# Performance work log

Hardware: AMD Instinct MI355X
Metric: run time of the kernel (lower is better)

Reference implementation:

```python
import jax, jax.numpy as jnp
import numpy as np

N = 10000        # nodes
E = 160000       # edges (avg degree 16)
MUL = 128        # channel multiplicity
A = 10           # node-attr (species one-hot) dim
RAD = 8          # radial bessel features
INV_SQRT3 = 0.5773502691896258  # CG coefficient for 1o x 1o -> 0e


def _mlp(x, Ws):
    # RadialMLP: linear layers with SiLU between, no activation on last
    for W in Ws[:-1]:
        x = jax.nn.silu(x @ W)
    return x @ Ws[-1]


def setup_inputs() -> dict:
    key = jax.random.key(0)
    ks = jax.random.split(key, 25)

    def g(k, shape):
        return jax.random.normal(k, shape, jnp.float32) / np.float32(np.sqrt(shape[0]))

    return {
        "node_attrs": jax.random.uniform(ks[0], (N, A), jnp.float32),
        "node_feats": jax.random.normal(ks[1], (N, 4 * MUL), jnp.float32),
        "edge_attrs": jax.random.normal(ks[2], (E, 4), jnp.float32),
        "edge_feats": jax.random.uniform(ks[3], (E, RAD), jnp.float32),
        "W_src": g(ks[5], (A, MUL)),
        "W_tgt": g(ks[6], (A, MUL)),
        "W_up0": g(ks[7], (MUL, MUL)),
        "W_up1": g(ks[8], (MUL, MUL)),
        "W_skip0": g(ks[9], (MUL, MUL)),
        "W_skip1": g(ks[10], (MUL, MUL)),
        "W_res0": g(ks[11], (MUL, 2 * MUL)),
        "W_res1": g(ks[12], (MUL, MUL)),
        "W_lin1_0": g(ks[13], (2 * MUL, 2 * MUL)),
        "W_lin1_1": g(ks[14], (2 * MUL, MUL)),
        "W_lin2_0": g(ks[15], (MUL, MUL)),
        "W_lin2_1": g(ks[16], (MUL, MUL)),
        "W_rad1": g(ks[17], (RAD + 2 * MUL, 64)),
        "W_rad2": g(ks[18], (64, 64)),
        "W_rad3": g(ks[19], (64, 64)),
        "W_rad4": g(ks[20], (64, 4 * MUL)),
        "W_den1": g(ks[21], (RAD + 2 * MUL, 64)),
        "W_den2": g(ks[22], (64, 1)),
        "alpha": jnp.ones((), jnp.float32),   # scaled by 20 inside (alpha = param * 20)
        "beta": jnp.zeros((), jnp.float32),
        "edge_index": jax.random.randint(ks[4], (E, 2), 0, N),
    }


def _forward(node_attrs, node_feats, edge_attrs, edge_feats,
             W_src, W_tgt, W_up0, W_up1, W_skip0, W_skip1, W_res0, W_res1,
             W_lin1_0, W_lin1_1, W_lin2_0, W_lin2_1,
             W_rad1, W_rad2, W_rad3, W_rad4, W_den1, W_den2,
             alpha, beta, edge_index):
    n = node_feats.shape[0]
    # split node feats into 128x0e scalars and 128x1o vectors (mul_ir layout)
    s = node_feats[:, :MUL]                           # [N, 128]
    v = node_feats[:, MUL:].reshape(n, MUL, 3)        # [N, 128, 3]

    # skip connection: Linear(node_feats_irreps -> hidden_irreps)
    sc_s = s @ W_skip0
    sc_v = jnp.einsum("nui,uv->nvi", v, W_skip1)
    sc = jnp.concatenate([sc_s, sc_v.reshape(n, -1)], axis=-1)  # [N, 512]

    # linear_up (node_feats -> edge_irreps) and linear_res (-> irreps_nonlin)
    up_s = s @ W_up0
    up_v = jnp.einsum("nui,uv->nvi", v, W_up1)
    res_s = s @ W_res0                                # [N, 256] (scalars + gates)
    res_v = jnp.einsum("nui,uv->nvi", v, W_res1)      # [N, 128, 3]

    # per-species scalar embeddings, gathered per edge
    src_emb = node_attrs @ W_src                      # [N, 128]
    tgt_emb = node_attrs @ W_tgt
    snd = edge_index[:, 0]
    rcv = edge_index[:, 1]
    aug = jnp.concatenate([edge_feats, src_emb[snd], tgt_emb[rcv]], axis=-1)  # [E, 264]

    # radial MLP -> per-edge tensor-product weights; density MLP
    tpw = _mlp(aug, [W_rad1, W_rad2, W_rad3, W_rad4])  # [E, 512]
    edge_density = jnp.tanh(_mlp(aug, [W_den1, W_den2]) ** 2)  # [E, 1]
    density = jax.ops.segment_sum(edge_density, rcv, num_segments=n)  # [N, 1]

    # equivariant tensor product (uvu, per-edge weights), lmax=1 CG paths
    xs = up_s[snd]                                    # [E, 128]
    xv = up_v[snd]                                    # [E, 128, 3]
    y0 = edge_attrs[:, :1]                            # [E, 1]
    y1 = edge_attrs[:, 1:4]                           # [E, 3]
    wA, wB, wC, wD = jnp.split(tpw, 4, axis=-1)
    mA = wA * xs * y0                                               # 0e x 0e -> 0e
    mD = wD * jnp.einsum("eui,ei->eu", xv, y1) * INV_SQRT3          # 1o x 1o -> 0e
    mB = (wB * xs)[:, :, None] * y1[:, None, :]                     # 0e x 1o -> 1o
    mC = wC[:, :, None] * xv * y0[:, :, None]                       # 1o x 0e -> 1o
    m_s = jnp.concatenate([mA, mD], axis=-1)          # [E, 256]
    m_v = jnp.concatenate([mB, mC], axis=1)           # [E, 256, 3]

    # scatter-add messages to receiver nodes
    msg_s = jax.ops.segment_sum(m_s, rcv, num_segments=n)  # [N, 256]
    msg_v = jax.ops.segment_sum(m_v, rcv, num_segments=n)  # [N, 256, 3]

    # linear_1 (irreps_mid -> irreps_nonlin), density normalization, residual
    msg_s = msg_s @ W_lin1_0                          # [N, 256]
    msg_v = jnp.einsum("nui,uv->nvi", msg_v, W_lin1_1)  # [N, 128, 3]
    denom = density * beta + alpha * 20.0             # [N, 1]
    msg_s = msg_s / denom + res_s
    msg_v = msg_v / denom[..., None] + res_v

    # equivariant gate nonlinearity: silu on scalars, sigmoid gates on vectors
    scal = jax.nn.silu(msg_s[:, :MUL])
    gate = jax.nn.sigmoid(msg_s[:, MUL:])
    vec = msg_v * gate[:, :, None]

    # linear_2 and reshape to [N, channels, (lmax+1)^2]
    out_s = scal @ W_lin2_0                           # [N, 128]
    out_v = jnp.einsum("nui,uv->nvi", vec, W_lin2_1)  # [N, 128, 3]
    message = jnp.concatenate([out_s[:, :, None], out_v], axis=-1)  # [N, 128, 4]
    return message, sc


def reference(node_attrs, node_feats, edge_attrs, edge_feats,
              W_src, W_tgt, W_up0, W_up1, W_skip0, W_skip1, W_res0, W_res1,
              W_lin1_0, W_lin1_1, W_lin2_0, W_lin2_1,
              W_rad1, W_rad2, W_rad3, W_rad4, W_den1, W_den2,
              alpha, beta, edge_index):
    return _forward(node_attrs, node_feats, edge_attrs, edge_feats,
                    W_src, W_tgt, W_up0, W_up1, W_skip0, W_skip1, W_res0, W_res1,
                    W_lin1_0, W_lin1_1, W_lin2_0, W_lin2_1,
                    W_rad1, W_rad2, W_rad3, W_rad4, W_den1, W_den2,
                    alpha, beta, edge_index)
```

## Files before the change

### kernel.cpp

```cpp
#include <hip/hip_runtime.h>
#include <math.h>

#define NN 10000
#define NE 160000
#define MUL 128
#define ADIM 10
#define RADF 8
#define HID 64
#define INV_SQRT3 0.57735026918962576f
#define NB64 157

typedef __attribute__((ext_vector_type(8))) short bf16x8;
typedef __attribute__((ext_vector_type(4))) float f32x4;

__device__ __forceinline__ float silu_f(float x){ return x / (1.0f + __expf(-x)); }
__device__ __forceinline__ float sigmoid_f(float x){ return 1.0f / (1.0f + __expf(-x)); }
__device__ __forceinline__ unsigned short f2b(float f){
  union{float f; unsigned u;} v; v.f=f;
  unsigned r = (v.u + 0x7fffu + ((v.u>>16)&1u))>>16;
  return (unsigned short)r;
}
__device__ __forceinline__ float b2f(unsigned short h){
  union{unsigned u; float f;} v; v.u = ((unsigned)h)<<16; return v.f;
}
__device__ __forceinline__ float b2f_lo(unsigned u){
  union{unsigned u; float f;} v; v.u = u<<16; return v.f;
}
__device__ __forceinline__ float b2f_hi(unsigned u){
  union{unsigned u; float f;} v; v.u = u & 0xffff0000u; return v.f;
}

__global__ __launch_bounds__(256) void k_wcomb(
    const float* __restrict__ Wsrc, const float* __restrict__ Wtgt,
    const float* __restrict__ Wr1, const float* __restrict__ Wd1,
    float* __restrict__ Wc){
  int tid = threadIdx.x;
  int m = tid>>6, c = tid&63;
  const float* WA = (m&1)? Wtgt : Wsrc;
  const float* WB = (m<2)? Wr1 : Wd1;
  int koff = (m&1)? 136 : 8;
  for (int a=0;a<ADIM;a++){
    float s=0.f;
    for (int k=0;k<128;k++) s += WA[a*128+k]*WB[(koff+k)*64+c];
    Wc[(m*ADIM+a)*64+c] = s;
  }
}

__global__ __launch_bounds__(256) void k_nodeemb(
    const float* __restrict__ attrs, const float* __restrict__ Wc,
    float* __restrict__ srP, float* __restrict__ trP,
    float* __restrict__ sdP, float* __restrict__ tdP){
  int idx = blockIdx.x*256 + threadIdx.x;
  if (idx >= NN*64) return;
  int n = idx>>6, c = idx&63;
  float s0=0,s1=0,s2=0,s3=0;
  #pragma unroll
  for (int a=0;a<ADIM;a++){
    float x = attrs[n*ADIM+a];
    s0 += x*Wc[(0*ADIM+a)*64+c];
    s1 += x*Wc[(1*ADIM+a)*64+c];
    s2 += x*Wc[(2*ADIM+a)*64+c];
    s3 += x*Wc[(3*ADIM+a)*64+c];
  }
  srP[idx]=s0; trP[idx]=s1; sdP[idx]=s2; tdP[idx]=s3;
}

__global__ __launch_bounds__(256) void k_feat_prep(
    const float* __restrict__ feats, unsigned short* __restrict__ fs16,
    unsigned short* __restrict__ fv16){
  int idx = blockIdx.x*256 + threadIdx.x;
  int n = idx >> 9, c = idx & 511;
  float v = feats[idx];
  if (c < 128) fs16[n*128 + c] = f2b(v);
  else {
    int q = c - 128; int u = q/3; int i = q - 3*u;
    fv16[((size_t)n*3 + i)*128 + u] = f2b(v);
  }
}

__global__ __launch_bounds__(256) void k_prep(
    const float* __restrict__ Wr2, const float* __restrict__ Wr3,
    const float* __restrict__ Wr4,
    const float* __restrict__ Wl10, const float* __restrict__ Wl11,
    const float* __restrict__ Wl20, const float* __restrict__ Wl21,
    const float* __restrict__ Wsk0, const float* __restrict__ Wup0, const float* __restrict__ Wres0,
    const float* __restrict__ Wsk1, const float* __restrict__ Wup1, const float* __restrict__ Wres1,
    unsigned short* __restrict__ WTr2, unsigned short* __restrict__ WTr3,
    unsigned short* __restrict__ WTr4,
    unsigned short* __restrict__ Wl10T, unsigned short* __restrict__ Wl11T,
    unsigned short* __restrict__ Wl20T, unsigned short* __restrict__ Wl21T,
    unsigned short* __restrict__ WnsT, unsigned short* __restrict__ WnvT){
  int idx = blockIdx.x*256 + threadIdx.x;
  if (idx < 4096){
    int j = idx; int n=j>>6, k=j&63;
    WTr2[j] = f2b(Wr2[k*64+n]);
  } else if (idx < 8192){
    int j = idx-4096; int n=j>>6, k=j&63;
    WTr3[j] = f2b(Wr3[k*64+n]);
  } else if (idx < 40960){
    int j = idx-8192; int n=j>>6, k=j&63;
    WTr4[j] = f2b(Wr4[k*512+n]);
  } else if (idx < 106496){
    int j = idx-40960; int n=j>>8, k=j&255;
    Wl10T[j] = f2b(Wl10[k*256+n]);
  } else if (idx < 139264){
    int j = idx-106496; int n=j>>8, k=j&255;
    Wl11T[j] = f2b(Wl11[k*128+n]);
  } else if (idx < 155648){
    int j = idx-139264; int n=j>>7, k=j&127;
    Wl20T[j] = f2b(Wl20[k*128+n]);
  } else if (idx < 172032){
    int j = idx-155648; int n=j>>7, k=j&127;
    Wl21T[j] = f2b(Wl21[k*128+n]);
  } else if (idx < 237568){
    int j = idx-172032; int n=j>>7, k=j&127;
    float v;
    if (n < 128)      v = Wsk0[k*128+n];
    else if (n < 256) v = Wup0[k*128+(n-128)];
    else              v = Wres0[k*256+(n-256)];
    WnsT[j] = f2b(v);
  } else if (idx < 286720){
    int j = idx-237568; int n=j>>7, k=j&127;
    float v;
    if (n < 128)      v = Wsk1[k*128+n];
    else if (n < 256) v = Wup1[k*128+(n-128)];
    else              v = Wres1[k*128+(n-256)];
    WnvT[j] = f2b(v);
  }
}

__global__ __launch_bounds__(256) void k_node_pre2(
    const unsigned short* __restrict__ fs16, const unsigned short* __restrict__ fv16,
    const unsigned short* __restrict__ WnsT, const unsigned short* __restrict__ WnvT,
    float* __restrict__ out_sc,
    unsigned* __restrict__ up_sp, unsigned* __restrict__ up_vp,
    float* __restrict__ res_s, float* __restrict__ res_v){
  __shared__ unsigned short fA[64][136];
  int nb = blockIdx.x*64;
  int c = blockIdx.y;
  int g, ntc;
  if (c < 4){ g=0; ntc=c; } else { g = 1 + (c-4)/3; ntc = (c-4)%3; }
  int tid = threadIdx.x;
  int w = tid>>6, l = tid&63, m0 = w*16, lr = l&15, lg = l>>4;
  for (int idx=tid; idx<64*16; idx+=256){
    int row = idx>>4, s8 = idx&15;
    int n = min(nb+row, NN-1);
    const unsigned short* src = (g==0) ? &fs16[(size_t)n*128 + s8*8]
                                       : &fv16[((size_t)n*3 + (g-1))*128 + s8*8];
    *(uint4*)&fA[row][s8*8] = *(const uint4*)src;
  }
  __syncthreads();
  const unsigned short* WT = ((g==0)? WnsT : WnvT) + (size_t)ntc*128*128;
  f32x4 acc[8];
  #pragma unroll
  for (int t=0;t<8;t++) acc[t]=(f32x4)(0.f);
  #pragma unroll
  for (int kb=0;kb<4;kb++){
    bf16x8 a = *(const bf16x8*)&fA[m0+lr][kb*32 + lg*8];
    #pragma unroll
    for (int t=0;t<8;t++){
      bf16x8 b = *(const bf16x8*)&WT[(size_t)(t*16+lr)*128 + kb*32 + lg*8];
      acc[t] = __builtin_amdgcn_mfma_f32_16x16x32_bf16(a, b, acc[t], 0,0,0);
    }
  }
  #pragma unroll
  for (int t=0;t<8;t++){
    #pragma unroll
    for (int r=0;r<4;r++){
      int col = (ntc*8+t)*16 + lr;
      int row = m0 + lg*4 + r;
      int n = nb + row;
      if (n < NN){
        float v = acc[t][r];
        if (g==0){
          if (col < 128)      out_sc[(size_t)n*512 + col] = v;
          else if (col < 256){
            int cc = col-128;
            ((unsigned short*)up_sp)[((size_t)n*64 + (cc&63))*2 + (cc>>6)] = f2b(v);
          } else              res_s[(size_t)n*256 + col-256] = v;
        } else {
          int i = g-1;
          if (col < 128)      out_sc[(size_t)n*512 + 128 + col*3 + i] = v;
          else if (col < 256){
            int cc = col-128;
            ((unsigned short*)up_vp)[(((size_t)n*3+i)*64 + (cc&63))*2 + (cc>>6)] = f2b(v);
          } else              res_v[((size_t)n*3+i)*128 + col-256] = v;
        }
      }
    }
  }
}

__global__ __launch_bounds__(256) void k_deg(const int* __restrict__ eidx, int* __restrict__ deg){
  int i = blockIdx.x*256+threadIdx.x;
  if (i<NE) atomicAdd(&deg[eidx[2*i+1]],1);
}
__global__ __launch_bounds__(256) void k_scan(const int* __restrict__ deg, int* __restrict__ offsets){
  __shared__ int part[256];
  int t = threadIdx.x; int base = t*40;
  int s=0;
  for (int k=0;k<40;k++){ int idx=base+k; if (idx<NN) s+=deg[idx]; }
  part[t]=s; __syncthreads();
  if (t==0){ int run=0; for (int i=0;i<256;i++){ int v=part[i]; part[i]=run; run+=v; } }
  __syncthreads();
  int run = part[t];
  for (int k=0;k<40;k++){
    int idx=base+k;
    if (idx<=NN) offsets[idx]=run;
    if (idx<NN) run+=deg[idx];
  }
}
__global__ __launch_bounds__(256) void k_fill(const int* __restrict__ eidx, const int* __restrict__ offsets,
                                              int* __restrict__ cursor, int* __restrict__ elist){
  int i = blockIdx.x*256+threadIdx.x;
  if (i<NE){ int r = eidx[2*i+1]; int p = atomicAdd(&cursor[r],1); elist[offsets[r]+p]=i; }
}

__global__ __launch_bounds__(256) void k_tpw(
    const int* __restrict__ elist, const int* __restrict__ eidx,
    const float* __restrict__ ef, const float* __restrict__ ea,
    const float* __restrict__ srP, const float* __restrict__ trP,
    const float* __restrict__ sdP, const float* __restrict__ tdP,
    const float* __restrict__ Wr1, const float* __restrict__ Wd1, const float* __restrict__ Wd2,
    const unsigned short* __restrict__ WTr2, const unsigned short* __restrict__ WTr3,
    const unsigned short* __restrict__ WTr4,
    const int* __restrict__ offsets, int nstart, int nend, int cap,
    unsigned* __restrict__ tpwp, float4* __restrict__ ybuf,
    int* __restrict__ sndbuf, float* __restrict__ densbuf){
  __shared__ unsigned short hA[64][72];
  __shared__ unsigned short hB[64][72];
  __shared__ unsigned short hC[64][72];
  __shared__ float efs[64][8];
  __shared__ int s_snd[64], s_rcv[64];
  int ebase = offsets[nstart];
  int eend  = min(offsets[nend], ebase + cap);
  int i0 = ebase + blockIdx.x*64;
  if (i0 >= eend) return;
  int nrows = min(64, eend - i0);
  int tid = threadIdx.x;
  int w = tid>>6, l = tid&63, m0 = w*16, lr = l&15, lg = l>>4;
  if (tid < 64){
    int ii = min(i0 + tid, eend-1);
    int e = elist[ii];
    int sn = eidx[2*e], rc = eidx[2*e+1];
    s_snd[tid]=sn; s_rcv[tid]=rc;
    if (tid < nrows){
      int li = i0 - ebase + tid;
      sndbuf[li] = sn;
      ybuf[li] = ((const float4*)ea)[e];
    }
  }
  if (tid < 128){
    int r = tid>>1, hf = tid&1;
    int e = elist[min(i0+r, eend-1)];
    *(float4*)&efs[r][hf*4] = *(const float4*)&ef[(size_t)e*8 + hf*4];
  }
  __syncthreads();
  {
    float wr[8], wd[8];
    #pragma unroll
    for (int k=0;k<8;k++){ wr[k]=Wr1[k*64+l]; wd[k]=Wd1[k*64+l]; }
    float wd2c = Wd2[l];
    #pragma unroll
    for (int j=0;j<16;j++){
      int r = m0+j;
      int sn = s_snd[r], rc = s_rcv[r];
      float h  = srP[sn*64+l] + trP[rc*64+l];
      float hd = sdP[sn*64+l] + tdP[rc*64+l];
      #pragma unroll
      for (int k=0;k<8;k++){ float ek=efs[r][k]; h += ek*wr[k]; hd += ek*wd[k]; }
      hA[r][l] = f2b(silu_f(h));
      float sv = silu_f(hd)*wd2c;
      #pragma unroll
      for (int m=32;m;m>>=1) sv += __shfl_xor(sv, m);
      if (l==0 && j+m0 < nrows) densbuf[i0 - ebase + r] = tanhf(sv*sv);
    }
  }
  f32x4 acc[4];
  #pragma unroll
  for (int nt=0;nt<4;nt++) acc[nt]=(f32x4)(0.f);
  for (int kb=0;kb<2;kb++){
    bf16x8 a = *(const bf16x8*)&hA[m0+lr][kb*32 + lg*8];
    #pragma unroll
    for (int nt=0;nt<4;nt++){
      bf16x8 b = *(const bf16x8*)&WTr2[(nt*16+lr)*64 + kb*32 + lg*8];
      acc[nt] = __builtin_amdgcn_mfma_f32_16x16x32_bf16(a, b, acc[nt], 0,0,0);
    }
  }
  #pragma unroll
  for (int nt=0;nt<4;nt++)
    #pragma unroll
    for (int r=0;r<4;r++)
      hB[m0+lg*4+r][nt*16+lr] = f2b(silu_f(acc[nt][r]));
  #pragma unroll
  for (int nt=0;nt<4;nt++) acc[nt]=(f32x4)(0.f);
  for (int kb=0;kb<2;kb++){
    bf16x8 a = *(const bf16x8*)&hB[m0+lr][kb*32 + lg*8];
    #pragma unroll
    for (int nt=0;nt<4;nt++){
      bf16x8 b = *(const bf16x8*)&WTr3[(nt*16+lr)*64 + kb*32 + lg*8];
      acc[nt] = __builtin_amdgcn_mfma_f32_16x16x32_bf16(a, b, acc[nt], 0,0,0);
    }
  }
  #pragma unroll
  for (int nt=0;nt<4;nt++)
    #pragma unroll
    for (int r=0;r<4;r++)
      hA[m0+lg*4+r][nt*16+lr] = f2b(silu_f(acc[nt][r]));
  int li0 = i0 - ebase + m0;
  (void)li0;
  for (int G=0; G<4; G++){
    f32x4 aE[4], aO[4];
    #pragma unroll
    for (int nt=0;nt<4;nt++){ aE[nt]=(f32x4)(0.f); aO[nt]=(f32x4)(0.f); }
    for (int kb=0;kb<2;kb++){
      bf16x8 a = *(const bf16x8*)&hA[m0+lr][kb*32 + lg*8];
      #pragma unroll
      for (int nt=0;nt<4;nt++){
        bf16x8 bE = *(const bf16x8*)&WTr4[((2*G)*64+nt*16+lr)*64 + kb*32 + lg*8];
        bf16x8 bO = *(const bf16x8*)&WTr4[((2*G+1)*64+nt*16+lr)*64 + kb*32 + lg*8];
        aE[nt] = __builtin_amdgcn_mfma_f32_16x16x32_bf16(a, bE, aE[nt], 0,0,0);
        aO[nt] = __builtin_amdgcn_mfma_f32_16x16x32_bf16(a, bO, aO[nt], 0,0,0);
      }
    }
    #pragma unroll
    for (int nt=0;nt<4;nt++)
      #pragma unroll
      for (int r=0;r<4;r++){
        hB[m0+lg*4+r][nt*16+lr] = f2b(aE[nt][r]);
        hC[m0+lg*4+r][nt*16+lr] = f2b(aO[nt][r]);
      }
    {
      int row = m0 + (l>>2), seg = l&3;
      if (row < nrows){
        const unsigned short* pb = &hB[row][seg*16];
        const unsigned short* pc = &hC[row][seg*16];
        unsigned o[16];
        #pragma unroll
        for (int t=0;t<16;t++) o[t] = (unsigned)pb[t] | ((unsigned)pc[t]<<16);
        size_t base = (size_t)(i0 - ebase + row)*256 + G*64 + seg*16;
        *(uint4*)&tpwp[base+0]  = *(uint4*)&o[0];
        *(uint4*)&tpwp[base+4]  = *(uint4*)&o[4];
        *(uint4*)&tpwp[base+8]  = *(uint4*)&o[8];
        *(uint4*)&tpwp[base+12] = *(uint4*)&o[12];
      }
    }
  }
}

__global__ __launch_bounds__(256) void k_gather(
    const unsigned* __restrict__ tpwp, const float4* __restrict__ ybuf,
    const int* __restrict__ sndbuf, const float* __restrict__ densbuf,
    const unsigned* __restrict__ up_sp, const unsigned* __restrict__ up_vp,
    const int* __restrict__ offsets, int nstart,
    unsigned short* __restrict__ msg_s16, unsigned short* __restrict__ msg_v16,
    float* __restrict__ density){
  int w = threadIdx.x>>6, l = threadIdx.x&63;
  int n = nstart + blockIdx.x*4 + w;
  if (n >= NN) return;
  int ebase = offsets[nstart];
  int s0 = offsets[n], s1 = offsets[n+1];
  float mA0=0,mA1=0,mD0=0,mD1=0;
  float mB00=0,mB01=0,mB10=0,mB11=0,mB20=0,mB21=0;
  float mC00=0,mC01=0,mC10=0,mC11=0,mC20=0,mC21=0;
  float dsum=0;
  #pragma unroll 2
  for (int i=s0;i<s1;++i){
    int li = i - ebase;
    int sn = sndbuf[li];
    float4 y = ybuf[li];
    dsum += densbuf[li];
    const unsigned* tp = tpwp + (size_t)li*256;
    unsigned uA = tp[l], uB = tp[64+l], uC = tp[128+l], uD = tp[192+l];
    float wA0=b2f_lo(uA), wA1=b2f_hi(uA);
    float wB0=b2f_lo(uB), wB1=b2f_hi(uB);
    float wC0=b2f_lo(uC), wC1=b2f_hi(uC);
    float wD0=b2f_lo(uD), wD1=b2f_hi(uD);
    unsigned us = up_sp[(size_t)sn*64 + l];
    float xs0=b2f_lo(us), xs1=b2f_hi(us);
    unsigned uv0 = up_vp[((size_t)sn*3+0)*64 + l];
    unsigned uv1 = up_vp[((size_t)sn*3+1)*64 + l];
    unsigned uv2 = up_vp[((size_t)sn*3+2)*64 + l];
    float xv00=b2f_lo(uv0), xv01=b2f_hi(uv0);
    float xv10=b2f_lo(uv1), xv11=b2f_hi(uv1);
    float xv20=b2f_lo(uv2), xv21=b2f_hi(uv2);
    mA0 += wA0*xs0*y.x; mA1 += wA1*xs1*y.x;
    float dot0 = xv00*y.y + xv10*y.z + xv20*y.w;
    float dot1 = xv01*y.y + xv11*y.z + xv21*y.w;
    mD0 += wD0*dot0; mD1 += wD1*dot1;
    float b0 = wB0*xs0, b1 = wB1*xs1;
    mB00 += b0*y.y; mB01 += b1*y.y;
    mB10 += b0*y.z; mB11 += b1*y.z;
    mB20 += b0*y.w; mB21 += b1*y.w;
    float c0 = wC0*y.x, c1 = wC1*y.x;
    mC00 += c0*xv00; mC01 += c1*xv01;
    mC10 += c0*xv10; mC11 += c1*xv11;
    mC20 += c0*xv20; mC21 += c1*xv21;
  }
  unsigned short* ms = msg_s16 + (size_t)n*256;
  ms[l]=f2b(mA0); ms[64+l]=f2b(mA1);
  ms[128+l]=f2b(mD0*INV_SQRT3); ms[192+l]=f2b(mD1*INV_SQRT3);
  unsigned short* mv = msg_v16 + (size_t)n*768;
  mv[l]=f2b(mB00);     mv[64+l]=f2b(mB01);  mv[128+l]=f2b(mC00); mv[192+l]=f2b(mC01);
  mv[256+l]=f2b(mB10); mv[320+l]=f2b(mB11); mv[384+l]=f2b(mC10); mv[448+l]=f2b(mC11);
  mv[512+l]=f2b(mB20); mv[576+l]=f2b(mB21); mv[640+l]=f2b(mC20); mv[704+l]=f2b(mC21);
  if (l==0) density[n]=dsum;
}

__global__ __launch_bounds__(256) void k_post1(
    const unsigned short* __restrict__ msg_s16, const unsigned short* __restrict__ msg_v16,
    const float* __restrict__ density,
    const float* __restrict__ res_s, const float* __restrict__ res_v,
    const unsigned short* __restrict__ Wl10T, const unsigned short* __restrict__ Wl11T,
    const float* __restrict__ alphap, const float* __restrict__ betap,
    unsigned short* __restrict__ scal16, unsigned short* __restrict__ gate16,
    unsigned short* __restrict__ vtmp16){
  __shared__ unsigned short sm[64][264];
  __shared__ float sden[64];
  int nb = blockIdx.x*64, y = blockIdx.y;
  int tid = threadIdx.x;
  int w = tid>>6, l = tid&63, m0 = w*16, lr = l&15, lg = l>>4;
  for (int idx=tid; idx<64*32; idx+=256){
    int row = idx>>5, s8 = idx&31;
    int n = min(nb+row, NN-1);
    const unsigned short* src = (y<2)? &msg_s16[(size_t)n*256 + s8*8]
                                     : &msg_v16[(size_t)n*768 + (y-2)*256 + s8*8];
    *(uint4*)&sm[row][s8*8] = *(const uint4*)src;
  }
  if (tid < 64){
    int n = min(nb+tid, NN-1);
    sden[tid] = density[n]*betap[0] + alphap[0]*20.0f;
  }
  __syncthreads();
  const unsigned short* BT = (y<2)? (Wl10T + (size_t)y*128*256) : Wl11T;
  f32x4 acc[8];
  #pragma unroll
  for (int t=0;t<8;t++) acc[t]=(f32x4)(0.f);
  for (int kb=0;kb<8;kb++){
    bf16x8 a = *(const bf16x8*)&sm[m0+lr][kb*32 + lg*8];
    #pragma unroll
    for (int t=0;t<8;t++){
      bf16x8 b = *(const bf16x8*)&BT[(size_t)(t*16+lr)*256 + kb*32 + lg*8];
      acc[t] = __builtin_amdgcn_mfma_f32_16x16x32_bf16(a, b, acc[t], 0,0,0);
    }
  }
  #pragma unroll
  for (int t=0;t<8;t++){
    #pragma unroll
    for (int r=0;r<4;r++){
      int col = t*16+lr;
      int row = m0 + lg*4 + r;
      int n = nb + row;
      if (n < NN){
        float v = acc[t][r]/sden[row];
        if (y==0){
          v += res_s[(size_t)n*256 + col];
          scal16[(size_t)n*128 + col] = f2b(silu_f(v));
        } else if (y==1){
          v += res_s[(size_t)n*256 + 128 + col];
          gate16[(size_t)n*128 + col] = f2b(sigmoid_f(v));
        } else {
          int i = y-2;
          v += res_v[((size_t)n*3+i)*128 + col];
          vtmp16[((size_t)i*NN + n)*128 + col] = f2b(v);
        }
      }
    }
  }
}

__global__ __launch_bounds__(256) void k_post2(
    const unsigned short* __restrict__ scal16, const unsigned short* __restrict__ gate16,
    const unsigned short* __restrict__ vtmp16,
    const unsigned short* __restrict__ Wl20T, const unsigned short* __restrict__ Wl21T,
    float* __restrict__ out_msg){
  __shared__ unsigned short sA[64][136];
  int nb = blockIdx.x*64, y = blockIdx.y;
  int tid = threadIdx.x;
  int w = tid>>6, l = tid&63, m0 = w*16, lr = l&15, lg = l>>4;
  for (int idx=tid; idx<64*16; idx+=256){
    int row = idx>>4, s8 = idx&15;
    int n = min(nb+row, NN-1);
    if (y==0){
      *(uint4*)&sA[row][s8*8] = *(const uint4*)&scal16[(size_t)n*128 + s8*8];
    } else {
      int i = y-1;
      uint4 va = *(const uint4*)&vtmp16[((size_t)i*NN + n)*128 + s8*8];
      uint4 vg = *(const uint4*)&gate16[(size_t)n*128 + s8*8];
      const unsigned short* pa = (const unsigned short*)&va;
      const unsigned short* pg = (const unsigned short*)&vg;
      unsigned short o[8];
      #pragma unroll
      for (int j=0;j<8;j++) o[j] = f2b(b2f(pa[j])*b2f(pg[j]));
      *(uint4*)&sA[row][s8*8] = *(const uint4*)o;
    }
  }
  __syncthreads();
  const unsigned short* BT = (y==0)? Wl20T : Wl21T;
  f32x4 acc[8];
  #pragma unroll
  for (int t=0;t<8;t++) acc[t]=(f32x4)(0.f);
  #pragma unroll
  for (int kb=0;kb<4;kb++){
    bf16x8 a = *(const bf16x8*)&sA[m0+lr][kb*32 + lg*8];
    #pragma unroll
    for (int t=0;t<8;t++){
      bf16x8 b = *(const bf16x8*)&BT[(size_t)(t*16+lr)*128 + kb*32 + lg*8];
      acc[t] = __builtin_amdgcn_mfma_f32_16x16x32_bf16(a, b, acc[t], 0,0,0);
    }
  }
  #pragma unroll
  for (int t=0;t<8;t++){
    #pragma unroll
    for (int r=0;r<4;r++){
      int col = t*16+lr;
      int n = nb + m0 + lg*4 + r;
      if (n < NN) out_msg[(size_t)n*512 + col*4 + y] = acc[t][r];
    }
  }
}

extern "C" void kernel_launch(void* const* d_in, const int* in_sizes, int n_in,
                              void* d_out, int out_size, void* d_ws, size_t ws_size,
                              hipStream_t stream){
  (void)in_sizes; (void)n_in; (void)out_size;
  const float* attrs = (const float*)d_in[0];
  const float* feats = (const float*)d_in[1];
  const float* ea    = (const float*)d_in[2];
  const float* ef    = (const float*)d_in[3];
  const float* Wsrc  = (const float*)d_in[4];
  const float* Wtgt  = (const float*)d_in[5];
  const float* Wup0  = (const float*)d_in[6];
  const float* Wup1  = (const float*)d_in[7];
  const float* Wsk0  = (const float*)d_in[8];
  const float* Wsk1  = (const float*)d_in[9];
  const float* Wres0 = (const float*)d_in[10];
  const float* Wres1 = (const float*)d_in[11];
  const float* Wl10  = (const float*)d_in[12];
  const float* Wl11  = (const float*)d_in[13];
  const float* Wl20  = (const float*)d_in[14];
  const float* Wl21  = (const float*)d_in[15];
  const float* Wr1   = (const float*)d_in[16];
  const float* Wr2   = (const float*)d_in[17];
  const float* Wr3   = (const float*)d_in[18];
  const float* Wr4   = (const float*)d_in[19];
  const float* Wd1   = (const float*)d_in[20];
  const float* Wd2   = (const float*)d_in[21];
  const float* alphap= (const float*)d_in[22];
  const float* betap = (const float*)d_in[23];
  const int*   eidx  = (const int*)d_in[24];

  const size_t fixed_bytes =
      (size_t)NN*256*2 + (size_t)NN*768*2 + (size_t)NN*256*4 + (size_t)NN*384*4 +
      (size_t)NN*4 + (size_t)NN*64*4 + (size_t)NN*192*4 +
      (size_t)NN*128*2 + (size_t)NN*384*2 +
      4*(size_t)NN*64*4 + 4*ADIM*64*4 + (size_t)NN*128*2 +
      (4096+4096+32768+65536+32768+16384+16384+65536+49152)*2 +
      (10240+10240+10256)*4 + (size_t)NE*4 + 64*256;
  int nchunk, npc, cap;
  if (fixed_bytes + (size_t)NE*1048 + 65536 <= ws_size){ nchunk=1; npc=NN;   cap=NE;    }
  else if (fixed_bytes + 81920ULL*1048 + 65536 <= ws_size){ nchunk=2; npc=5000; cap=81920; }
  else { nchunk=4; npc=2500; cap=44032; }

  char* p = (char*)d_ws;
  auto alloc = [&](size_t bytes)->char*{ char* r=p; p += (bytes+255)&~(size_t)255; return r; };
  unsigned* tpwp  = (unsigned*)alloc((size_t)cap*256*4);
  unsigned short* msg_s16 = (unsigned short*)alloc((size_t)NN*256*2);
  unsigned short* msg_v16 = (unsigned short*)alloc((size_t)NN*768*2);
  float*  res_s   = (float*)alloc((size_t)NN*256*4);
  float*  res_v   = (float*)alloc((size_t)NN*384*4);
  float*  density = (float*)alloc((size_t)NN*4);
  float4* ybuf    = (float4*)alloc((size_t)cap*16);
  float*  densbuf = (float*)alloc((size_t)cap*4);
  int*    sndbuf  = (int*)alloc((size_t)cap*4);
  unsigned* up_sp = (unsigned*)alloc((size_t)NN*64*4);
  unsigned* up_vp = (unsigned*)alloc((size_t)NN*192*4);
  unsigned short* fs16 = (unsigned short*)alloc((size_t)NN*128*2);
  unsigned short* fv16 = (unsigned short*)alloc((size_t)NN*384*2);
  float* srP = (float*)alloc((size_t)NN*64*4);
  float* trP = (float*)alloc((size_t)NN*64*4);
  float* sdP = (float*)alloc((size_t)NN*64*4);
  float* tdP = (float*)alloc((size_t)NN*64*4);
  float* Wc  = (float*)alloc(4*ADIM*64*4);
  unsigned short* gate16 = (unsigned short*)alloc((size_t)NN*128*2);
  unsigned short* WTr2 = (unsigned short*)alloc(4096*2);
  unsigned short* WTr3 = (unsigned short*)alloc(4096*2);
  unsigned short* WTr4 = (unsigned short*)alloc(32768*2);
  unsigned short* Wl10T = (unsigned short*)alloc(65536*2);
  unsigned short* Wl11T = (unsigned short*)alloc(32768*2);
  unsigned short* Wl20T = (unsigned short*)alloc(16384*2);
  unsigned short* Wl21T = (unsigned short*)alloc(16384*2);
  unsigned short* WnsT  = (unsigned short*)alloc(65536*2);
  unsigned short* WnvT  = (unsigned short*)alloc(49152*2);
  int* deg     = (int*)alloc(10240*4);
  int* cursor  = (int*)alloc(10240*4);
  int* offsets = (int*)alloc(10256*4);
  int* elist   = (int*)alloc((size_t)NE*4);

  unsigned short* scal16 = fs16;
  unsigned short* vtmp16 = fv16;

  float* out_msg = (float*)d_out;
  float* out_sc  = out_msg + (size_t)NN*512;

  hipMemsetAsync(deg, 0, 2*10240*sizeof(int), stream);

  k_wcomb<<<1, 256, 0, stream>>>(Wsrc, Wtgt, Wr1, Wd1, Wc);
  k_prep<<<1120, 256, 0, stream>>>(Wr2, Wr3, Wr4, Wl10, Wl11, Wl20, Wl21,
                                   Wsk0, Wup0, Wres0, Wsk1, Wup1, Wres1,
                                   WTr2, WTr3, WTr4,
                                   Wl10T, Wl11T, Wl20T, Wl21T, WnsT, WnvT);
  k_nodeemb<<<(NN*64+255)/256, 256, 0, stream>>>(attrs, Wc, srP, trP, sdP, tdP);
  k_feat_prep<<<NN*512/256, 256, 0, stream>>>(feats, fs16, fv16);
  k_node_pre2<<<dim3(NB64,13), 256, 0, stream>>>(fs16, fv16, WnsT, WnvT,
                                                 out_sc, up_sp, up_vp, res_s, res_v);
  k_deg<<<(NE+255)/256, 256, 0, stream>>>(eidx, deg);
  k_scan<<<1, 256, 0, stream>>>(deg, offsets);
  k_fill<<<(NE+255)/256, 256, 0, stream>>>(eidx, offsets, cursor, elist);

  int tpw_blocks = (cap+63)/64;
  for (int c=0; c<nchunk; ++c){
    k_tpw<<<tpw_blocks, 256, 0, stream>>>(elist, eidx, ef, ea,
                                          srP, trP, sdP, tdP,
                                          Wr1, Wd1, Wd2, WTr2, WTr3, WTr4,
                                          offsets, c*npc, (c+1)*npc, cap,
                                          tpwp, ybuf, sndbuf, densbuf);
    k_gather<<<npc/4, 256, 0, stream>>>(tpwp, ybuf, sndbuf, densbuf, up_sp, up_vp,
                                        offsets, c*npc, msg_s16, msg_v16, density);
  }

  k_post1<<<dim3(NB64,5), 256, 0, stream>>>(msg_s16, msg_v16, density, res_s, res_v,
                                            Wl10T, Wl11T, alphap, betap,
                                            scal16, gate16, vtmp16);
  k_post2<<<dim3(NB64,4), 256, 0, stream>>>(scal16, gate16, vtmp16,
                                            Wl20T, Wl21T, out_msg);
}
```

Baseline: 464.1 us.

## Interleave per-node and per-edge buffers for vector loads in edge kernels

Node embedding projections are interleaved into two float2-packed arrays, one for sender terms and one for receiver terms. The up-projected node features are packed into one 16-byte record per node and channel pair, and the per-edge tensor-product weights are written in a channel-interleaved layout. Together these let the gather kernel fetch each edge's weights and sender features with one uint4 load apiece instead of eight scattered 32-bit loads, and the radial MLP kernel now writes its output straight from registers without a shared-memory staging buffer. The weight-combine kernel is folded into the prep kernel, which removes one launch but runs its serial 128-term loop inside a single extra block.

```diff
diff --git a/kernel.cpp b/kernel.cpp
--- a/kernel.cpp
+++ b/kernel.cpp
@@ -30,26 +30,9 @@
   union{unsigned u; float f;} v; v.u = u & 0xffff0000u; return v.f;
 }
 
-__global__ __launch_bounds__(256) void k_wcomb(
-    const float* __restrict__ Wsrc, const float* __restrict__ Wtgt,
-    const float* __restrict__ Wr1, const float* __restrict__ Wd1,
-    float* __restrict__ Wc){
-  int tid = threadIdx.x;
-  int m = tid>>6, c = tid&63;
-  const float* WA = (m&1)? Wtgt : Wsrc;
-  const float* WB = (m<2)? Wr1 : Wd1;
-  int koff = (m&1)? 136 : 8;
-  for (int a=0;a<ADIM;a++){
-    float s=0.f;
-    for (int k=0;k<128;k++) s += WA[a*128+k]*WB[(koff+k)*64+c];
-    Wc[(m*ADIM+a)*64+c] = s;
-  }
-}
-
 __global__ __launch_bounds__(256) void k_nodeemb(
     const float* __restrict__ attrs, const float* __restrict__ Wc,
-    float* __restrict__ srP, float* __restrict__ trP,
-    float* __restrict__ sdP, float* __restrict__ tdP){
+    float* __restrict__ pA, float* __restrict__ pB){
   int idx = blockIdx.x*256 + threadIdx.x;
   if (idx >= NN*64) return;
   int n = idx>>6, c = idx&63;
@@ -62,7 +45,10 @@
     s2 += x*Wc[(2*ADIM+a)*64+c];
     s3 += x*Wc[(3*ADIM+a)*64+c];
   }
-  srP[idx]=s0; trP[idx]=s1; sdP[idx]=s2; tdP[idx]=s3;
+  pA[(size_t)n*128 + c*2 + 0] = s0;
+  pA[(size_t)n*128 + c*2 + 1] = s2;
+  pB[(size_t)n*128 + c*2 + 0] = s1;
+  pB[(size_t)n*128 + c*2 + 1] = s3;
 }
 
 __global__ __launch_bounds__(256) void k_feat_prep(
@@ -85,11 +71,14 @@
     const float* __restrict__ Wl20, const float* __restrict__ Wl21,
     const float* __restrict__ Wsk0, const float* __restrict__ Wup0, const float* __restrict__ Wres0,
     const float* __restrict__ Wsk1, const float* __restrict__ Wup1, const float* __restrict__ Wres1,
+    const float* __restrict__ Wsrc, const float* __restrict__ Wtgt,
+    const float* __restrict__ Wr1, const float* __restrict__ Wd1,
     unsigned short* __restrict__ WTr2, unsigned short* __restrict__ WTr3,
     unsigned short* __restrict__ WTr4,
     unsigned short* __restrict__ Wl10T, unsigned short* __restrict__ Wl11T,
     unsigned short* __restrict__ Wl20T, unsigned short* __restrict__ Wl21T,
-    unsigned short* __restrict__ WnsT, unsigned short* __restrict__ WnvT){
+    unsigned short* __restrict__ WnsT, unsigned short* __restrict__ WnvT,
+    float* __restrict__ Wc){
   int idx = blockIdx.x*256 + threadIdx.x;
   if (idx < 4096){
     int j = idx; int n=j>>6, k=j&63;
@@ -126,6 +115,17 @@
     else if (n < 256) v = Wup1[k*128+(n-128)];
     else              v = Wres1[k*128+(n-256)];
     WnvT[j] = f2b(v);
+  } else if (idx < 286976){
+    int j = idx - 286720;
+    int m = j>>6, c = j&63;
+    const float* WA = (m&1)? Wtgt : Wsrc;
+    const float* WB = (m<2)? Wr1 : Wd1;
+    int koff = (m&1)? 136 : 8;
+    for (int a=0;a<ADIM;a++){
+      float s=0.f;
+      for (int k=0;k<128;k++) s += WA[a*128+k]*WB[(koff+k)*64+c];
+      Wc[(m*ADIM+a)*64+c] = s;
+    }
   }
 }
 
@@ -133,7 +133,7 @@
     const unsigned short* __restrict__ fs16, const unsigned short* __restrict__ fv16,
     const unsigned short* __restrict__ WnsT, const unsigned short* __restrict__ WnvT,
     float* __restrict__ out_sc,
-    unsigned* __restrict__ up_sp, unsigned* __restrict__ up_vp,
+    unsigned short* __restrict__ upk16,
     float* __restrict__ res_s, float* __restrict__ res_v){
   __shared__ unsigned short fA[64][136];
   int nb = blockIdx.x*64;
@@ -176,14 +176,14 @@
           if (col < 128)      out_sc[(size_t)n*512 + col] = v;
           else if (col < 256){
             int cc = col-128;
-            ((unsigned short*)up_sp)[((size_t)n*64 + (cc&63))*2 + (cc>>6)] = f2b(v);
+            upk16[(size_t)n*512 + (cc&63)*8 + (cc>>6)] = f2b(v);
           } else              res_s[(size_t)n*256 + col-256] = v;
         } else {
           int i = g-1;
           if (col < 128)      out_sc[(size_t)n*512 + 128 + col*3 + i] = v;
           else if (col < 256){
             int cc = col-128;
-            ((unsigned short*)up_vp)[(((size_t)n*3+i)*64 + (cc&63))*2 + (cc>>6)] = f2b(v);
+            upk16[(size_t)n*512 + (cc&63)*8 + (1+i)*2 + (cc>>6)] = f2b(v);
           } else              res_v[((size_t)n*3+i)*128 + col-256] = v;
         }
       }
@@ -219,8 +219,7 @@
 __global__ __launch_bounds__(256) void k_tpw(
     const int* __restrict__ elist, const int* __restrict__ eidx,
     const float* __restrict__ ef, const float* __restrict__ ea,
-    const float* __restrict__ srP, const float* __restrict__ trP,
-    const float* __restrict__ sdP, const float* __restrict__ tdP,
+    const float* __restrict__ pA, const float* __restrict__ pB,
     const float* __restrict__ Wr1, const float* __restrict__ Wd1, const float* __restrict__ Wd2,
     const unsigned short* __restrict__ WTr2, const unsigned short* __restrict__ WTr3,
     const unsigned short* __restrict__ WTr4,
@@ -229,7 +228,6 @@
     int* __restrict__ sndbuf, float* __restrict__ densbuf){
   __shared__ unsigned short hA[64][72];
   __shared__ unsigned short hB[64][72];
-  __shared__ unsigned short hC[64][72];
   __shared__ float efs[64][8];
   __shared__ int s_snd[64], s_rcv[64];
   int ebase = offsets[nstart];
@@ -265,20 +263,23 @@
     for (int j=0;j<16;j++){
       int r = m0+j;
       int sn = s_snd[r], rc = s_rcv[r];
-      float h  = srP[sn*64+l] + trP[rc*64+l];
-      float hd = sdP[sn*64+l] + tdP[rc*64+l];
+      float2 av = *(const float2*)&pA[(size_t)sn*128 + l*2];
+      float2 bv = *(const float2*)&pB[(size_t)rc*128 + l*2];
+      float h  = av.x + bv.x;
+      float hd = av.y + bv.y;
       #pragma unroll
       for (int k=0;k<8;k++){ float ek=efs[r][k]; h += ek*wr[k]; hd += ek*wd[k]; }
       hA[r][l] = f2b(silu_f(h));
       float sv = silu_f(hd)*wd2c;
       #pragma unroll
       for (int m=32;m;m>>=1) sv += __shfl_xor(sv, m);
-      if (l==0 && j+m0 < nrows) densbuf[i0 - ebase + r] = tanhf(sv*sv);
+      if (l==0 && r < nrows) densbuf[i0 - ebase + r] = tanhf(sv*sv);
     }
   }
   f32x4 acc[4];
   #pragma unroll
   for (int nt=0;nt<4;nt++) acc[nt]=(f32x4)(0.f);
+  #pragma unroll
   for (int kb=0;kb<2;kb++){
     bf16x8 a = *(const bf16x8*)&hA[m0+lr][kb*32 + lg*8];
     #pragma unroll
@@ -294,6 +295,7 @@
       hB[m0+lg*4+r][nt*16+lr] = f2b(silu_f(acc[nt][r]));
   #pragma unroll
   for (int nt=0;nt<4;nt++) acc[nt]=(f32x4)(0.f);
+  #pragma unroll
   for (int kb=0;kb<2;kb++){
     bf16x8 a = *(const bf16x8*)&hB[m0+lr][kb*32 + lg*8];
     #pragma unroll
@@ -307,43 +309,30 @@
     #pragma unroll
     for (int r=0;r<4;r++)
       hA[m0+lg*4+r][nt*16+lr] = f2b(silu_f(acc[nt][r]));
-  int li0 = i0 - ebase + m0;
-  (void)li0;
-  for (int G=0; G<4; G++){
-    f32x4 aE[4], aO[4];
-    #pragma unroll
-    for (int nt=0;nt<4;nt++){ aE[nt]=(f32x4)(0.f); aO[nt]=(f32x4)(0.f); }
-    for (int kb=0;kb<2;kb++){
-      bf16x8 a = *(const bf16x8*)&hA[m0+lr][kb*32 + lg*8];
+  int erow0 = i0 - ebase;
+  #pragma unroll
+  for (int nt=0; nt<4; nt++){
+    unsigned pvv[4][4];
+    #pragma unroll
+    for (int G=0; G<4; G++){
+      f32x4 aE=(f32x4)(0.f), aO=(f32x4)(0.f);
       #pragma unroll
-      for (int nt=0;nt<4;nt++){
+      for (int kb=0; kb<2; kb++){
+        bf16x8 a  = *(const bf16x8*)&hA[m0+lr][kb*32 + lg*8];
         bf16x8 bE = *(const bf16x8*)&WTr4[((2*G)*64+nt*16+lr)*64 + kb*32 + lg*8];
         bf16x8 bO = *(const bf16x8*)&WTr4[((2*G+1)*64+nt*16+lr)*64 + kb*32 + lg*8];
-        aE[nt] = __builtin_amdgcn_mfma_f32_16x16x32_bf16(a, bE, aE[nt], 0,0,0);
-        aO[nt] = __builtin_amdgcn_mfma_f32_16x16x32_bf16(a, bO, aO[nt], 0,0,0);
+        aE = __builtin_amdgcn_mfma_f32_16x16x32_bf16(a, bE, aE, 0,0,0);
+        aO = __builtin_amdgcn_mfma_f32_16x16x32_bf16(a, bO, aO, 0,0,0);
       }
-    }
-    #pragma unroll
-    for (int nt=0;nt<4;nt++)
       #pragma unroll
-      for (int r=0;r<4;r++){
-        hB[m0+lg*4+r][nt*16+lr] = f2b(aE[nt][r]);
-        hC[m0+lg*4+r][nt*16+lr] = f2b(aO[nt][r]);
-      }
-    {
-      int row = m0 + (l>>2), seg = l&3;
-      if (row < nrows){
-        const unsigned short* pb = &hB[row][seg*16];
-        const unsigned short* pc = &hC[row][seg*16];
-        unsigned o[16];
-        #pragma unroll
-        for (int t=0;t<16;t++) o[t] = (unsigned)pb[t] | ((unsigned)pc[t]<<16);
-        size_t base = (size_t)(i0 - ebase + row)*256 + G*64 + seg*16;
-        *(uint4*)&tpwp[base+0]  = *(uint4*)&o[0];
-        *(uint4*)&tpwp[base+4]  = *(uint4*)&o[4];
-        *(uint4*)&tpwp[base+8]  = *(uint4*)&o[8];
-        *(uint4*)&tpwp[base+12] = *(uint4*)&o[12];
-      }
+      for (int r=0;r<4;r++)
+        pvv[r][G] = (unsigned)f2b(aE[r]) | ((unsigned)f2b(aO[r])<<16);
+    }
+    #pragma unroll
+    for (int r=0;r<4;r++){
+      int row = m0 + lg*4 + r;
+      if (row < nrows)
+        *(uint4*)&tpwp[(size_t)(erow0+row)*256 + (nt*16+lr)*4] = *(uint4*)&pvv[r][0];
     }
   }
 }
@@ -351,7 +340,7 @@
 __global__ __launch_bounds__(256) void k_gather(
     const unsigned* __restrict__ tpwp, const float4* __restrict__ ybuf,
     const int* __restrict__ sndbuf, const float* __restrict__ densbuf,
-    const unsigned* __restrict__ up_sp, const unsigned* __restrict__ up_vp,
+    const uint4* __restrict__ upk4,
     const int* __restrict__ offsets, int nstart,
     unsigned short* __restrict__ msg_s16, unsigned short* __restrict__ msg_v16,
     float* __restrict__ density){
@@ -370,20 +359,16 @@
     int sn = sndbuf[li];
     float4 y = ybuf[li];
     dsum += densbuf[li];
-    const unsigned* tp = tpwp + (size_t)li*256;
-    unsigned uA = tp[l], uB = tp[64+l], uC = tp[128+l], uD = tp[192+l];
-    float wA0=b2f_lo(uA), wA1=b2f_hi(uA);
-    float wB0=b2f_lo(uB), wB1=b2f_hi(uB);
-    float wC0=b2f_lo(uC), wC1=b2f_hi(uC);
-    float wD0=b2f_lo(uD), wD1=b2f_hi(uD);
-    unsigned us = up_sp[(size_t)sn*64 + l];
-    float xs0=b2f_lo(us), xs1=b2f_hi(us);
-    unsigned uv0 = up_vp[((size_t)sn*3+0)*64 + l];
-    unsigned uv1 = up_vp[((size_t)sn*3+1)*64 + l];
-    unsigned uv2 = up_vp[((size_t)sn*3+2)*64 + l];
-    float xv00=b2f_lo(uv0), xv01=b2f_hi(uv0);
-    float xv10=b2f_lo(uv1), xv11=b2f_hi(uv1);
-    float xv20=b2f_lo(uv2), xv21=b2f_hi(uv2);
+    uint4 tq = *(const uint4*)&tpwp[(size_t)li*256 + l*4];
+    uint4 uq = upk4[(size_t)sn*64 + l];
+    float wA0=b2f_lo(tq.x), wA1=b2f_hi(tq.x);
+    float wB0=b2f_lo(tq.y), wB1=b2f_hi(tq.y);
+    float wC0=b2f_lo(tq.z), wC1=b2f_hi(tq.z);
+    float wD0=b2f_lo(tq.w), wD1=b2f_hi(tq.w);
+    float xs0=b2f_lo(uq.x), xs1=b2f_hi(uq.x);
+    float xv00=b2f_lo(uq.y), xv01=b2f_hi(uq.y);
+    float xv10=b2f_lo(uq.z), xv11=b2f_hi(uq.z);
+    float xv20=b2f_lo(uq.w), xv21=b2f_hi(uq.w);
     mA0 += wA0*xs0*y.x; mA1 += wA1*xs1*y.x;
     float dot0 = xv00*y.y + xv10*y.z + xv20*y.w;
     float dot1 = xv01*y.y + xv11*y.z + xv21*y.w;
@@ -551,11 +536,8 @@
   const int*   eidx  = (const int*)d_in[24];
 
   const size_t fixed_bytes =
-      (size_t)NN*256*2 + (size_t)NN*768*2 + (size_t)NN*256*4 + (size_t)NN*384*4 +
-      (size_t)NN*4 + (size_t)NN*64*4 + (size_t)NN*192*4 +
-      (size_t)NN*128*2 + (size_t)NN*384*2 +
-      4*(size_t)NN*64*4 + 4*ADIM*64*4 + (size_t)NN*128*2 +
-      (4096+4096+32768+65536+32768+16384+16384+65536+49152)*2 +
+      (size_t)NN*(512 + 1536 + 1024 + 1536 + 4 + 1024 + 256 + 768 + 512 + 512 + 256) +
+      (size_t)286976*2 + 4*ADIM*64*4 +
       (10240+10240+10256)*4 + (size_t)NE*4 + 64*256;
   int nchunk, npc, cap;
   if (fixed_bytes + (size_t)NE*1048 + 65536 <= ws_size){ nchunk=1; npc=NN;   cap=NE;    }
@@ -573,14 +555,11 @@
   float4* ybuf    = (float4*)alloc((size_t)cap*16);
   float*  densbuf = (float*)alloc((size_t)cap*4);
   int*    sndbuf  = (int*)alloc((size_t)cap*4);
-  unsigned* up_sp = (unsigned*)alloc((size_t)NN*64*4);
-  unsigned* up_vp = (unsigned*)alloc((size_t)NN*192*4);
+  uint4*  upk     = (uint4*)alloc((size_t)NN*64*16);
   unsigned short* fs16 = (unsigned short*)alloc((size_t)NN*128*2);
   unsigned short* fv16 = (unsigned short*)alloc((size_t)NN*384*2);
-  float* srP = (float*)alloc((size_t)NN*64*4);
-  float* trP = (float*)alloc((size_t)NN*64*4);
-  float* sdP = (float*)alloc((size_t)NN*64*4);
-  float* tdP = (float*)alloc((size_t)NN*64*4);
+  float* pA = (float*)alloc((size_t)NN*128*4);
+  float* pB = (float*)alloc((size_t)NN*128*4);
   float* Wc  = (float*)alloc(4*ADIM*64*4);
   unsigned short* gate16 = (unsigned short*)alloc((size_t)NN*128*2);
   unsigned short* WTr2 = (unsigned short*)alloc(4096*2);
@@ -605,27 +584,26 @@
 
   hipMemsetAsync(deg, 0, 2*10240*sizeof(int), stream);
 
-  k_wcomb<<<1, 256, 0, stream>>>(Wsrc, Wtgt, Wr1, Wd1, Wc);
-  k_prep<<<1120, 256, 0, stream>>>(Wr2, Wr3, Wr4, Wl10, Wl11, Wl20, Wl21,
+  k_prep<<<1121, 256, 0, stream>>>(Wr2, Wr3, Wr4, Wl10, Wl11, Wl20, Wl21,
                                    Wsk0, Wup0, Wres0, Wsk1, Wup1, Wres1,
+                                   Wsrc, Wtgt, Wr1, Wd1,
                                    WTr2, WTr3, WTr4,
-                                   Wl10T, Wl11T, Wl20T, Wl21T, WnsT, WnvT);
-  k_nodeemb<<<(NN*64+255)/256, 256, 0, stream>>>(attrs, Wc, srP, trP, sdP, tdP);
+                                   Wl10T, Wl11T, Wl20T, Wl21T, WnsT, WnvT, Wc);
+  k_nodeemb<<<(NN*64+255)/256, 256, 0, stream>>>(attrs, Wc, pA, pB);
   k_feat_prep<<<NN*512/256, 256, 0, stream>>>(feats, fs16, fv16);
   k_node_pre2<<<dim3(NB64,13), 256, 0, stream>>>(fs16, fv16, WnsT, WnvT,
-                                                 out_sc, up_sp, up_vp, res_s, res_v);
+                                                 out_sc, (unsigned short*)upk, res_s, res_v);
   k_deg<<<(NE+255)/256, 256, 0, stream>>>(eidx, deg);
   k_scan<<<1, 256, 0, stream>>>(deg, offsets);
   k_fill<<<(NE+255)/256, 256, 0, stream>>>(eidx, offsets, cursor, elist);
 
   int tpw_blocks = (cap+63)/64;
   for (int c=0; c<nchunk; ++c){
-    k_tpw<<<tpw_blocks, 256, 0, stream>>>(elist, eidx, ef, ea,
-                                          srP, trP, sdP, tdP,
+    k_tpw<<<tpw_blocks, 256, 0, stream>>>(elist, eidx, ef, ea, pA, pB,
                                           Wr1, Wd1, Wd2, WTr2, WTr3, WTr4,
                                           offsets, c*npc, (c+1)*npc, cap,
                                           tpwp, ybuf, sndbuf, densbuf);
-    k_gather<<<npc/4, 256, 0, stream>>>(tpwp, ybuf, sndbuf, densbuf, up_sp, up_vp,
+    k_gather<<<npc/4, 256, 0, stream>>>(tpwp, ybuf, sndbuf, densbuf, upk,
                                         offsets, c*npc, msg_s16, msg_v16, density);
   }
 
```

Result: faster. 446.2 us (-3.9%).
